# Kernel tuning notes

Measured on AMD Instinct MI355X. Metric: run time of the kernel, lower is better.

The kernel has to match this reference:

```python
import jax, jax.numpy as jnp
import numpy as np
from jax import lax

DIM = 180; NH = 6; WH = 16; WW = 16; MH = 8; MW = 8
HD = DIM // (2 * NH)  # 15, head dim; also the (non-sqrt) scale
RMS_EPS = 1.1920929e-07  # torch.finfo(float32).eps (RMSNorm eps=None)

def _conv(x, w, b, pad):
    # x: NHWC, w: HWIO
    return lax.conv_general_dilated(x, w, (1, 1), [(pad, pad), (pad, pad)],
                                    dimension_numbers=('NHWC', 'HWIO', 'NHWC')) + b

def _lrelu(x):
    return jnp.where(x >= 0, x, 0.2 * x)

def _ln(x, w, b, eps=1e-5):
    m = x.mean(-1, keepdims=True)
    v = jnp.mean((x - m) ** 2, -1, keepdims=True)
    return (x - m) / jnp.sqrt(v + eps) * w + b

def _forward(x, dfe_w1, dfe_b1, dfe_w2, dfe_b2, dfe_w3, dfe_b3, dfe_lw, dfe_lb,
             sl_w, sl_b, pos_pw, pos_pb, ln1w, ln1b, l1w, l1b, ln2w, ln2b,
             l2w, l2b, ln3w, ln3b, l3w, l3b, proj_w, proj_b, norm_w):
    B, C, H, W = x.shape
    xh = jnp.transpose(x, (0, 2, 3, 1))  # NHWC
    shortcut = xh
    # DFE: conv branch gated by 1x1 linear branch
    h = _lrelu(_conv(xh, dfe_w1, dfe_b1, 0))
    h = _lrelu(_conv(h, dfe_w2, dfe_b2, 1))
    h = _conv(h, dfe_w3, dfe_b3, 0)
    qv = h * _conv(xh, dfe_lw, dfe_lb, 0)  # (B,H,W,C)
    # window partition
    L = WH * WW
    qv = qv.reshape(B, H // WH, WH, W // WW, WW, C).transpose(0, 1, 3, 2, 4, 5).reshape(-1, L, C)
    Bw = qv.shape[0]
    qv = qv.reshape(Bw, L, 2, NH, HD).transpose(2, 0, 3, 1, 4)
    q, v = qv[0], qv[1]  # (Bw, NH, L, HD)
    # spatial linear projection of v: downsample window -> base window
    rH, rW = WH // MH, WW // MW
    vp = v.reshape(Bw, NH, MH, rH, MW, rW, HD).transpose(0, 1, 2, 4, 6, 3, 5)
    vp = vp.reshape(Bw, NH, MH * MW, HD, rH * rW)
    vp = ((vp @ sl_w) + sl_b)[..., 0]  # (Bw, NH, mapL, HD)
    corr = jnp.einsum('bhlc,bhmc->bhlm', q, vp) / HD  # (Bw, NH, L, mapL)
    # dynamic relative position bias
    bh = jnp.arange(1 - WH, WH, dtype=jnp.float32)
    bw = jnp.arange(1 - WW, WW, dtype=jnp.float32)
    biases = jnp.stack(jnp.meshgrid(bh, bw, indexing='ij')).reshape(2, -1).T  # (nb, 2)
    p = biases @ pos_pw + pos_pb
    p = jax.nn.relu(_ln(p, ln1w, ln1b)) @ l1w + l1b
    p = jax.nn.relu(_ln(p, ln2w, ln2b)) @ l2w + l2b
    pos = jax.nn.relu(_ln(p, ln3w, ln3b)) @ l3w + l3b  # (nb, NH)
    coords = jnp.stack(jnp.meshgrid(jnp.arange(WH), jnp.arange(WW), indexing='ij')).reshape(2, -1)
    rel = coords[:, :, None] - coords[:, None, :]  # (2, L, L)
    idx = (rel[0] + WH - 1) * (2 * WW - 1) + (rel[1] + WW - 1)  # (L, L)
    rpb = pos[idx.reshape(-1)].reshape(L, MH, rH, MW, rW, NH)
    rpb = rpb.transpose(0, 1, 3, 5, 2, 4).reshape(L, MH * MW, NH, rH * rW).mean(-1)
    rpb = rpb.transpose(2, 0, 1)  # (NH, L, mapL)
    corr = corr + rpb[None]
    xs = jnp.einsum('bhlm,bhmc->bhlc', corr, vp).transpose(0, 2, 1, 3).reshape(Bw, L, NH * HD)
    # channel self-correlation
    qc = q.transpose(0, 2, 1, 3).reshape(Bw, L, NH * HD)
    vc = v.transpose(0, 2, 1, 3).reshape(Bw, L, NH * HD)
    cmap = jnp.einsum('blc,bld->bcd', qc, vc) / L  # (Bw, C/2, C/2)
    xc = jnp.einsum('bcd,bld->blc', cmap, vc)  # (Bw, L, C/2)
    # window reverse
    def wrev(win):
        c = win.shape[-1]
        return win.reshape(B, H // WH, W // WW, WH, WW, c).transpose(0, 1, 3, 2, 4, 5).reshape(B, H, W, c)
    xs = wrev(xs.reshape(Bw, WH, WW, NH * HD))
    xc = wrev(xc.reshape(Bw, WH, WW, NH * HD))
    y = jnp.concatenate([xs, xc], -1)  # (B, H, W, C)
    y = y @ proj_w + proj_b
    y = y * (1.0 / jnp.sqrt(jnp.mean(y * y, -1, keepdims=True) + RMS_EPS)) * norm_w
    y = shortcut + y
    return jnp.transpose(y, (0, 3, 1, 2))


def setup_inputs() -> dict:
    key = jax.random.key(0)
    ks = iter(jax.random.split(key, 32))
    def rn(shape, s=0.05):
        return jax.random.normal(next(ks), shape, jnp.float32) * s
    inp = {}
    inp['x'] = jax.random.normal(next(ks), (4, 180, 256, 256), jnp.float32)
    inp['dfe_w1'] = rn((1, 1, 180, 36)); inp['dfe_b1'] = rn((36,))
    inp['dfe_w2'] = rn((3, 3, 36, 36)); inp['dfe_b2'] = rn((36,))
    inp['dfe_w3'] = rn((1, 1, 36, 180)); inp['dfe_b3'] = rn((180,))
    inp['dfe_lw'] = rn((1, 1, 180, 180)); inp['dfe_lb'] = rn((180,))
    inp['sl_w'] = rn((4, 1)); inp['sl_b'] = rn((1,))
    inp['pos_pw'] = rn((2, 11)); inp['pos_pb'] = rn((11,))
    inp['ln1w'] = jnp.ones((11,)); inp['ln1b'] = jnp.zeros((11,))
    inp['l1w'] = rn((11, 11)); inp['l1b'] = rn((11,))
    inp['ln2w'] = jnp.ones((11,)); inp['ln2b'] = jnp.zeros((11,))
    inp['l2w'] = rn((11, 11)); inp['l2b'] = rn((11,))
    inp['ln3w'] = jnp.ones((11,)); inp['ln3b'] = jnp.zeros((11,))
    inp['l3w'] = rn((11, 6)); inp['l3b'] = rn((6,))
    inp['proj_w'] = rn((180, 180)); inp['proj_b'] = rn((180,))
    inp['norm_w'] = jnp.ones((180,))
    return inp


def reference(x, dfe_w1, dfe_b1, dfe_w2, dfe_b2, dfe_w3, dfe_b3, dfe_lw, dfe_lb,
              sl_w, sl_b, pos_pw, pos_pb, ln1w, ln1b, l1w, l1b, ln2w, ln2b,
              l2w, l2b, ln3w, ln3b, l3w, l3b, proj_w, proj_b, norm_w):
    return _forward(x, dfe_w1, dfe_b1, dfe_w2, dfe_b2, dfe_w3, dfe_b3, dfe_lw, dfe_lb,
                    sl_w, sl_b, pos_pw, pos_pb, ln1w, ln1b, l1w, l1b, ln2w, ln2b,
                    l2w, l2b, ln3w, ln3b, l3w, l3b, proj_w, proj_b, norm_w)
```

## Files before the change

kernel.cpp:

```cpp
#include <hip/hip_runtime.h>
#include <stdint.h>

typedef unsigned short u16;
typedef unsigned int   u32;

#define HW 65536

typedef __bf16 bf16x8 __attribute__((ext_vector_type(8)));
typedef float  f32x4  __attribute__((ext_vector_type(4)));

static __device__ __forceinline__ float bf2f(u16 h) {
    u32 u = ((u32)h) << 16;
    return __builtin_bit_cast(float, u);
}
static __device__ __forceinline__ u16 f2bf(float f) {
    u32 u = __builtin_bit_cast(u32, f);
    u += 0x7fffu + ((u >> 16) & 1u);
    return (u16)(u >> 16);
}
static __device__ __forceinline__ void bf2x2(u32 u, float& a, float& b) {
    a = __builtin_bit_cast(float, u << 16);
    b = __builtin_bit_cast(float, u & 0xffff0000u);
}
static __device__ __forceinline__ f32x4 mfma16(bf16x8 a, bf16x8 b, f32x4 c) {
    return __builtin_amdgcn_mfma_f32_16x16x32_bf16(a, b, c, 0, 0, 0);
}

static __device__ __forceinline__ void lnrelu11(float* p, const float* __restrict__ w,
                                                const float* __restrict__ b) {
    float m = 0.f;
    #pragma unroll
    for (int k = 0; k < 11; k++) m += p[k];
    m *= (1.0f / 11.0f);
    float v = 0.f;
    #pragma unroll
    for (int k = 0; k < 11; k++) { float d = p[k] - m; v = fmaf(d, d, v); }
    v *= (1.0f / 11.0f);
    float r = 1.0f / sqrtf(v + 1e-5f);
    #pragma unroll
    for (int k = 0; k < 11; k++) {
        float t = (p[k] - m) * r * w[k] + b[k];
        p[k] = t > 0.f ? t : 0.f;
    }
}

__global__ __launch_bounds__(1024) void k_pos(
    const float* __restrict__ pw, const float* __restrict__ pb,
    const float* __restrict__ ln1w, const float* __restrict__ ln1b,
    const float* __restrict__ l1w, const float* __restrict__ l1b,
    const float* __restrict__ ln2w, const float* __restrict__ ln2b,
    const float* __restrict__ l2w, const float* __restrict__ l2b,
    const float* __restrict__ ln3w, const float* __restrict__ ln3b,
    const float* __restrict__ l3w, const float* __restrict__ l3b,
    float* __restrict__ pos)
{
    int i = threadIdx.x;
    if (i >= 961) return;
    float b0 = (float)(i / 31) - 15.0f;
    float b1 = (float)(i % 31) - 15.0f;
    float p[11], t[11];
    #pragma unroll
    for (int j = 0; j < 11; j++) p[j] = b0 * pw[j] + b1 * pw[11 + j] + pb[j];
    lnrelu11(p, ln1w, ln1b);
    #pragma unroll
    for (int j = 0; j < 11; j++) {
        float s = l1b[j];
        #pragma unroll
        for (int k = 0; k < 11; k++) s = fmaf(p[k], l1w[k * 11 + j], s);
        t[j] = s;
    }
    lnrelu11(t, ln2w, ln2b);
    #pragma unroll
    for (int j = 0; j < 11; j++) {
        float s = l2b[j];
        #pragma unroll
        for (int k = 0; k < 11; k++) s = fmaf(t[k], l2w[k * 11 + j], s);
        p[j] = s;
    }
    lnrelu11(p, ln3w, ln3b);
    #pragma unroll
    for (int h = 0; h < 6; h++) {
        float s = l3b[h];
        #pragma unroll
        for (int k = 0; k < 11; k++) s = fmaf(p[k], l3w[k * 6 + h], s);
        pos[i * 6 + h] = s;
    }
}

__global__ __launch_bounds__(256) void k_rpb(const float* __restrict__ pos,
                                             float* __restrict__ rpb)
{
    int g = blockIdx.x * 256 + threadIdx.x;
    if (g >= 6 * 256 * 64) return;
    int h = g >> 14;
    int l = (g >> 6) & 255;
    int m = g & 63;
    int yl = l >> 4, xl = l & 15;
    int my = m >> 3, mx = m & 7;
    float s = 0.f;
    #pragma unroll
    for (int ry = 0; ry < 2; ry++) {
        #pragma unroll
        for (int rx = 0; rx < 2; rx++) {
            int y2 = my * 2 + ry, x2 = mx * 2 + rx;
            int idx = (yl - y2 + 15) * 31 + (xl - x2 + 15);
            s += pos[idx * 6 + h];
        }
    }
    rpb[g] = 0.25f * s;
}

__global__ __launch_bounds__(256) void k_conv1(const float* __restrict__ x,
                                               const float* __restrict__ w,
                                               const float* __restrict__ b,
                                               u16* __restrict__ h1)
{
    int pix = blockIdx.x * 256 + threadIdx.x;
    int bb = pix >> 16, sp = pix & 65535;
    float acc[36];
    #pragma unroll
    for (int j = 0; j < 36; j++) acc[j] = b[j];
    const float* xp = x + (size_t)bb * 180 * HW + sp;
    for (int c = 0; c < 180; c++) {
        float xv = xp[(size_t)c * HW];
        #pragma unroll
        for (int j = 0; j < 36; j++) acc[j] = fmaf(xv, w[c * 36 + j], acc[j]);
    }
    u16* hp = h1 + (size_t)bb * 36 * HW + sp;
    #pragma unroll
    for (int j = 0; j < 36; j++) {
        float v = acc[j];
        v = v >= 0.f ? v : 0.2f * v;
        hp[(size_t)j * HW] = f2bf(v);
    }
}

__global__ __launch_bounds__(256) void k_conv3(const u16* __restrict__ h1,
                                               const float* __restrict__ w,
                                               const float* __restrict__ b,
                                               u16* __restrict__ h2)
{
    int tx = threadIdx.x, ty = threadIdx.y;
    int x0 = blockIdx.x * 16 + tx;
    int y0 = blockIdx.y * 16 + ty;
    int bb = blockIdx.z;
    float acc[36];
    #pragma unroll
    for (int j = 0; j < 36; j++) acc[j] = b[j];
    const u16* base = h1 + (size_t)bb * 36 * HW;
    for (int ky = 0; ky < 3; ky++) {
        int yy = y0 + ky - 1;
        if (yy < 0 || yy >= 256) continue;
        for (int kx = 0; kx < 3; kx++) {
            int xx = x0 + kx - 1;
            if (xx < 0 || xx >= 256) continue;
            const u16* ip = base + yy * 256 + xx;
            const float* wp = w + ((ky * 3 + kx) * 36) * 36;
            for (int c = 0; c < 36; c++) {
                float v = bf2f(ip[(size_t)c * HW]);
                #pragma unroll
                for (int j = 0; j < 36; j++) acc[j] = fmaf(v, wp[c * 36 + j], acc[j]);
            }
        }
    }
    u16* op = h2 + (size_t)bb * 36 * HW + y0 * 256 + x0;
    #pragma unroll
    for (int j = 0; j < 36; j++) {
        float v = acc[j];
        v = v >= 0.f ? v : 0.2f * v;
        op[(size_t)j * HW] = f2bf(v);
    }
}

__global__ __launch_bounds__(256) void k_wgprep(const float* __restrict__ lw,
                                                const float* __restrict__ w3,
                                                u16* __restrict__ gwh,
                                                u16* __restrict__ gwl,
                                                u16* __restrict__ cwh,
                                                u16* __restrict__ cwl)
{
    int gidx = blockIdx.x * 256 + threadIdx.x;
    if (gidx < 36864) {
        int oc = gidx / 192, k = gidx % 192;
        float v = (oc < 180 && k < 180) ? lw[k * 180 + oc] : 0.f;
        u16 h = f2bf(v);
        float lo = v - bf2f(h);
        gwh[gidx] = h;
        gwl[gidx] = f2bf(lo);
    } else {
        int r = gidx - 36864;
        int oc = r / 64, k = r % 64;
        float v = (oc < 180 && k < 36) ? w3[k * 180 + oc] : 0.f;
        u16 h = f2bf(v);
        float lo = v - bf2f(h);
        cwh[r] = h;
        cwl[r] = f2bf(lo);
    }
}

__global__ __launch_bounds__(256) void k_gate(const u16* __restrict__ h2,
                                              const float* __restrict__ x,
                                              const u16* __restrict__ gwh,
                                              const u16* __restrict__ gwl,
                                              const u16* __restrict__ cwh,
                                              const u16* __restrict__ cwl,
                                              const float* __restrict__ b3,
                                              const float* __restrict__ lb,
                                              u16* __restrict__ qvT)
{
    __shared__ __align__(16) float xs[180 * 64];
    __shared__ __align__(16) u16  hs[36 * 64];
    int t = threadIdx.x;
    int lane = t & 63;
    int g = __builtin_amdgcn_readfirstlane(t >> 6);
    int m = lane & 15, q = lane >> 4;
    int blk = blockIdx.x;
    int w  = blk >> 2;
    int lq = blk & 3;
    int bb = w >> 8, wy = (w >> 4) & 15, wx = w & 15;
    int ocb = g * 48;
    int y0 = wy * 16 + lq * 4;
    int xc0 = wx * 16;
    const float* xb = x + (size_t)bb * 180 * HW;
    const u16*  hb = h2 + (size_t)bb * 36 * HW;

    for (int s = g; s < 45; s += 4) {
        int c = s * 4 + (lane >> 4);
        int swz = (c >> 3) & 1;
        int pp = (lane & 15) ^ (swz << 2);
        int p0 = pp * 4;
        int prow = p0 >> 4, pcol = p0 & 15;
        const float* gp = xb + (size_t)c * HW + (y0 + prow) * 256 + xc0 + pcol;
        __builtin_amdgcn_global_load_lds(
            (const __attribute__((address_space(1))) void*)gp,
            (__attribute__((address_space(3))) void*)(xs + s * 256),
            16, 0, 0);
    }
    for (int idx = t; idx < 288; idx += 256) {
        int c = idx >> 3, j = idx & 7;
        int p0 = j * 8;
        int prow = p0 >> 4, pcol = p0 & 15;
        uint4 v = *(const uint4*)(hb + (size_t)c * HW + (y0 + prow) * 256 + xc0 + pcol);
        int swz = (c >> 3) & 1;
        *(uint4*)(hs + c * 64 + (p0 ^ (swz << 4))) = v;
    }
    __syncthreads();

    f32x4 accG[3][4], accC[3][4];
    #pragma unroll
    for (int mt = 0; mt < 3; mt++)
        #pragma unroll
        for (int pt = 0; pt < 4; pt++) {
            f32x4 z = {0.f, 0.f, 0.f, 0.f};
            accG[mt][pt] = z;
            accC[mt][pt] = z;
        }

    #pragma unroll 2
    for (int ks = 0; ks < 6; ks++) {
        bf16x8 Bh[4], Bl[4];
        #pragma unroll
        for (int pt = 0; pt < 4; pt++)
            #pragma unroll
            for (int j = 0; j < 8; j++) {
                int c = ks * 32 + q * 8 + j;
                if (c > 179) c = 179;
                int p = pt * 16 + m;
                float v = xs[c * 64 + (p ^ (((c >> 3) & 1) << 4))];
                __bf16 hi = (__bf16)v;
                Bh[pt][j] = hi;
                Bl[pt][j] = (__bf16)(v - (float)hi);
            }
        #pragma unroll
        for (int mt = 0; mt < 3; mt++) {
            bf16x8 Ah = *(const bf16x8*)(gwh + (size_t)(ocb + mt * 16 + m) * 192 + ks * 32 + q * 8);
            bf16x8 Al = *(const bf16x8*)(gwl + (size_t)(ocb + mt * 16 + m) * 192 + ks * 32 + q * 8);
            #pragma unroll
            for (int pt = 0; pt < 4; pt++) {
                accG[mt][pt] = mfma16(Ah, Bh[pt], accG[mt][pt]);
                accG[mt][pt] = mfma16(Al, Bh[pt], accG[mt][pt]);
                accG[mt][pt] = mfma16(Ah, Bl[pt], accG[mt][pt]);
            }
        }
    }

    #pragma unroll
    for (int ks = 0; ks < 2; ks++) {
        bf16x8 B[4];
        #pragma unroll
        for (int pt = 0; pt < 4; pt++)
            #pragma unroll
            for (int j = 0; j < 8; j++) {
                int c = ks * 32 + q * 8 + j;
                if (c > 35) c = 35;
                int p = pt * 16 + m;
                B[pt][j] = __builtin_bit_cast(__bf16, hs[c * 64 + (p ^ (((c >> 3) & 1) << 4))]);
            }
        #pragma unroll
        for (int mt = 0; mt < 3; mt++) {
            bf16x8 Ah = *(const bf16x8*)(cwh + (size_t)(ocb + mt * 16 + m) * 64 + ks * 32 + q * 8);
            bf16x8 Al = *(const bf16x8*)(cwl + (size_t)(ocb + mt * 16 + m) * 64 + ks * 32 + q * 8);
            #pragma unroll
            for (int pt = 0; pt < 4; pt++) {
                accC[mt][pt] = mfma16(Ah, B[pt], accC[mt][pt]);
                accC[mt][pt] = mfma16(Al, B[pt], accC[mt][pt]);
            }
        }
    }

    u16* qw = qvT + (size_t)w * 180 * 256 + lq * 64 + m;
    #pragma unroll
    for (int mt = 0; mt < 3; mt++)
        #pragma unroll
        for (int r = 0; r < 4; r++) {
            int oc = ocb + mt * 16 + q * 4 + r;
            if (oc < 180) {
                float bc = b3[oc], bg = lb[oc];
                #pragma unroll
                for (int pt = 0; pt < 4; pt++) {
                    float ah = accC[mt][pt][r] + bc;
                    float al = accG[mt][pt][r] + bg;
                    qw[(size_t)oc * 256 + pt * 16] = f2bf(ah * al);
                }
            }
        }
}

__global__ __launch_bounds__(256) void k_spat(const u16* __restrict__ qvT,
                                              const float* __restrict__ rpb,
                                              const float* __restrict__ slw,
                                              const float* __restrict__ slb,
                                              u16* __restrict__ yp)
{
    __shared__ __align__(16) float vp[6144];
    int w = blockIdx.x;
    int bb = w >> 8, wy = (w >> 4) & 15, wx = w & 15;
    int t = threadIdx.x;
    int lane = t & 63, wv = t >> 6;
    const u16* qw = qvT + (size_t)w * 180 * 256;
    float s0 = slw[0], s1 = slw[1], s2 = slw[2], s3 = slw[3], sb = slb[0];
    for (int o = t; o < 384; o += 256) vp[(o >> 6) * 1024 + (o & 63) * 16 + 15] = 0.f;
    for (int it = 0; it < 23; it++) {
        int p = wv + it * 4;
        if (p < 90) {
            int mm = lane;
            int l0 = (mm >> 3) * 32 + (mm & 7) * 2;
            const u16* rp2 = qw + (size_t)(90 + p) * 256;
            float s = sb + s0 * bf2f(rp2[l0]) + s1 * bf2f(rp2[l0 + 1])
                         + s2 * bf2f(rp2[l0 + 16]) + s3 * bf2f(rp2[l0 + 17]);
            vp[(p / 15) * 1024 + mm * 16 + (p % 15)] = s;
        }
    }
    __syncthreads();
    int l = t;
    size_t pixl = (size_t)((bb * 256 + wy * 16 + (l >> 4)) * 256 + wx * 16 + (l & 15));
    u16* op = yp + pixl * 192;
    ((u32*)op)[45] = 0u; ((u32*)op)[46] = 0u; ((u32*)op)[47] = 0u;
    for (int h = 0; h < 6; h++) {
        float q[16];
        #pragma unroll
        for (int d = 0; d < 15; d++) q[d] = bf2f(qw[(size_t)(h * 15 + d) * 256 + l]);
        q[15] = 0.f;
        float acc[16];
        #pragma unroll
        for (int d = 0; d < 16; d++) acc[d] = 0.f;
        const float* rp = rpb + ((h * 256 + l) << 6);
        const float4* vph = (const float4*)(vp + (h << 10));
        for (int m0 = 0; m0 < 64; m0 += 4) {
            float ra[4];
            *(float4*)ra = *(const float4*)(rp + m0);
            #pragma unroll
            for (int mm = 0; mm < 4; mm++) {
                int m = m0 + mm;
                float wvv[16];
                ((float4*)wvv)[0] = vph[m * 4 + 0];
                ((float4*)wvv)[1] = vph[m * 4 + 1];
                ((float4*)wvv)[2] = vph[m * 4 + 2];
                ((float4*)wvv)[3] = vph[m * 4 + 3];
                float s = 0.f;
                #pragma unroll
                for (int d2 = 0; d2 < 16; d2++) s = fmaf(q[d2], wvv[d2], s);
                s = s * (1.0f / 15.0f) + ra[mm];
                #pragma unroll
                for (int d2 = 0; d2 < 16; d2++) acc[d2] = fmaf(s, wvv[d2], acc[d2]);
            }
        }
        #pragma unroll
        for (int d = 0; d < 15; d++) op[h * 15 + d] = f2bf(acc[d]);
    }
}

__global__ __launch_bounds__(256) void k_chan(const u16* __restrict__ qvT,
                                              u16* __restrict__ yp)
{
    __shared__ __align__(16) u16 cm[96 * 104];
    __shared__ __align__(16) u16 xcb[128 * 104];
    int w = blockIdx.x;
    int bb = w >> 8, wy = (w >> 4) & 15, wx = w & 15;
    int t = threadIdx.x;
    int lane = t & 63, wv = t >> 6;
    int m = lane & 15, quad = lane >> 4;
    const u16* qw = qvT + (size_t)w * 180 * 256;

    int ct0 = (wv & 1) * 3, dt0 = (wv >> 1) * 3;
    f32x4 acc[3][3];
    #pragma unroll
    for (int i = 0; i < 3; i++)
        #pragma unroll
        for (int j = 0; j < 3; j++) {
            f32x4 z = {0.f, 0.f, 0.f, 0.f};
            acc[i][j] = z;
        }
    #pragma unroll
    for (int ks = 0; ks < 8; ks++) {
        bf16x8 A[3], B[3];
        #pragma unroll
        for (int i = 0; i < 3; i++)
            A[i] = *(const bf16x8*)(qw + (size_t)((ct0 + i) * 16 + m) * 256 + ks * 32 + quad * 8);
        #pragma unroll
        for (int j = 0; j < 3; j++) {
            int d = (dt0 + j) * 16 + m;
            int dd = d > 89 ? 89 : d;
            B[j] = *(const bf16x8*)(qw + (size_t)(90 + dd) * 256 + ks * 32 + quad * 8);
        }
        #pragma unroll
        for (int i = 0; i < 3; i++)
            #pragma unroll
            for (int j = 0; j < 3; j++)
                acc[i][j] = mfma16(A[i], B[j], acc[i][j]);
    }
    #pragma unroll
    for (int i = 0; i < 3; i++)
        #pragma unroll
        for (int j = 0; j < 3; j++)
            #pragma unroll
            for (int r = 0; r < 4; r++)
                cm[((ct0 + i) * 16 + quad * 4 + r) * 104 + (dt0 + j) * 16 + m] =
                    f2bf(acc[i][j][r] * (1.0f / 256.0f));
    __syncthreads();
    if (t < 96) {
        u32* z = (u32*)(cm + t * 104 + 90);
        z[0] = 0; z[1] = 0; z[2] = 0;
    }
    __syncthreads();

    int base_pix = (bb * 256 + wy * 16) * 256 + wx * 16;
    const __bf16* qwb = (const __bf16*)qw;
    for (int half = 0; half < 2; half++) {
        #pragma unroll
        for (int i = 0; i < 2; i++) {
            int ltl = wv * 2 + i;
            int lt = half * 8 + ltl;
            bf16x8 A[3];
            #pragma unroll
            for (int ks = 0; ks < 3; ks++) {
                const __bf16* colp = qwb + lt * 16 + m;
                #pragma unroll
                for (int j2 = 0; j2 < 8; j2++) {
                    int d = ks * 32 + quad * 8 + j2;
                    int dd = d > 89 ? 89 : d;
                    A[ks][j2] = colp[(size_t)(90 + dd) * 256];
                }
            }
            for (int ct = 0; ct < 6; ct++) {
                f32x4 c4 = {0.f, 0.f, 0.f, 0.f};
                #pragma unroll
                for (int ks = 0; ks < 3; ks++) {
                    bf16x8 B = *(const bf16x8*)(cm + (ct * 16 + m) * 104 + ks * 32 + quad * 8);
                    c4 = mfma16(A[ks], B, c4);
                }
                #pragma unroll
                for (int r = 0; r < 4; r++)
                    xcb[(ltl * 16 + quad * 4 + r) * 104 + ct * 16 + m] = f2bf(c4[r]);
            }
        }
        __syncthreads();
        #pragma unroll
        for (int it = 0; it < 6; it++) {
            int gg = t + it * 256;
            int lrow = gg / 12, seg = gg % 12;
            int l = half * 128 + lrow;
            int pix = base_pix + (l >> 4) * 256 + (l & 15);
            *(uint4*)(yp + (size_t)pix * 192 + 96 + seg * 8) =
                *(const uint4*)(xcb + lrow * 104 + seg * 8);
        }
        __syncthreads();
    }
}

__global__ __launch_bounds__(256) void k_wprep(const float* __restrict__ pjw,
                                               u16* __restrict__ whiT,
                                               u16* __restrict__ wloT)
{
    int g = blockIdx.x * 256 + threadIdx.x;
    int oc = g / 192, k = g % 192;
    int kp = -1;
    if (k < 90) kp = k;
    else if (k >= 96 && k <= 185) kp = k - 6;
    float v = (kp >= 0 && oc < 180) ? pjw[kp * 180 + oc] : 0.f;
    u16 h = f2bf(v);
    float lo = v - bf2f(h);
    whiT[g] = h;
    wloT[g] = f2bf(lo);
}

__global__ __launch_bounds__(256) void k_proj(const u16* __restrict__ yp,
                                              const float* __restrict__ x,
                                              const u16* __restrict__ whiT,
                                              const u16* __restrict__ wloT,
                                              const float* __restrict__ pb,
                                              const float* __restrict__ nw,
                                              float* __restrict__ out)
{
    __shared__ __align__(16) float st[96 * 68];
    __shared__ float part[4][4][16];
    int t = threadIdx.x;
    int lane = t & 63;
    int g = __builtin_amdgcn_readfirstlane(t >> 6);
    int m = lane & 15, q = lane >> 4;
    int pix0 = blockIdx.x * 64;
    int ocbase = g * 48;

    f32x4 acc[3][4];
    #pragma unroll
    for (int mt = 0; mt < 3; mt++)
        #pragma unroll
        for (int pt = 0; pt < 4; pt++) {
            f32x4 z = {0.f, 0.f, 0.f, 0.f};
            acc[mt][pt] = z;
        }

    const u16* bbase = yp + (size_t)pix0 * 192;
    #pragma unroll 2
    for (int ks = 0; ks < 6; ks++) {
        bf16x8 B[4];
        #pragma unroll
        for (int pt = 0; pt < 4; pt++)
            B[pt] = *(const bf16x8*)(bbase + (size_t)(pt * 16 + m) * 192 + ks * 32 + q * 8);
        #pragma unroll
        for (int mt = 0; mt < 3; mt++) {
            bf16x8 Ah = *(const bf16x8*)(whiT + (size_t)(ocbase + mt * 16 + m) * 192 + ks * 32 + q * 8);
            bf16x8 Al = *(const bf16x8*)(wloT + (size_t)(ocbase + mt * 16 + m) * 192 + ks * 32 + q * 8);
            #pragma unroll
            for (int pt = 0; pt < 4; pt++) {
                acc[mt][pt] = mfma16(Ah, B[pt], acc[mt][pt]);
                acc[mt][pt] = mfma16(Al, B[pt], acc[mt][pt]);
            }
        }
    }

    float pbv[3][4], nwv[3][4];
    #pragma unroll
    for (int mt = 0; mt < 3; mt++)
        #pragma unroll
        for (int r = 0; r < 4; r++) {
            int oc = ocbase + mt * 16 + q * 4 + r;
            bool ok = oc < 180;
            pbv[mt][r] = ok ? pb[oc] : 0.f;
            nwv[mt][r] = ok ? nw[oc] : 0.f;
        }
    float ss[4] = {0.f, 0.f, 0.f, 0.f};
    #pragma unroll
    for (int mt = 0; mt < 3; mt++)
        #pragma unroll
        for (int pt = 0; pt < 4; pt++)
            #pragma unroll
            for (int r = 0; r < 4; r++) {
                float y = acc[mt][pt][r] + pbv[mt][r];
                acc[mt][pt][r] = y;
                ss[pt] = fmaf(y, y, ss[pt]);
            }
    #pragma unroll
    for (int pt = 0; pt < 4; pt++) {
        ss[pt] += __shfl_xor(ss[pt], 16);
        ss[pt] += __shfl_xor(ss[pt], 32);
    }
    if (q == 0) {
        #pragma unroll
        for (int pt = 0; pt < 4; pt++) part[g][pt][m] = ss[pt];
    }
    __syncthreads();
    float scale[4];
    #pragma unroll
    for (int pt = 0; pt < 4; pt++) {
        float tot = part[0][pt][m] + part[1][pt][m] + part[2][pt][m] + part[3][pt][m];
        scale[pt] = 1.0f / sqrtf(tot * (1.0f / 180.0f) + 1.1920929e-7f);
    }
    #pragma unroll
    for (int mt = 0; mt < 3; mt++)
        #pragma unroll
        for (int pt = 0; pt < 4; pt++)
            #pragma unroll
            for (int r = 0; r < 4; r++)
                acc[mt][pt][r] = acc[mt][pt][r] * scale[pt] * nwv[mt][r];

    int bb = pix0 >> 16, sp0 = pix0 & 65535;
    const float* xb = x + (size_t)bb * 180 * HW + sp0;
    float* ob = out + (size_t)bb * 180 * HW + sp0;
    #pragma unroll
    for (int ph = 0; ph < 2; ph++) {
        if ((g >> 1) == ph) {
            int rb = (g & 1) * 48;
            #pragma unroll
            for (int mt = 0; mt < 3; mt++)
                #pragma unroll
                for (int r = 0; r < 4; r++) {
                    int row = rb + mt * 16 + q * 4 + r;
                    #pragma unroll
                    for (int pt = 0; pt < 4; pt++)
                        st[row * 68 + pt * 16 + m] = acc[mt][pt][r];
                }
        }
        __syncthreads();
        int nch = ph ? 1344 : 1536;
        for (int i = t; i < nch; i += 256) {
            int row = i >> 4, j = i & 15;
            int oc = ph * 96 + row;
            f32x4 d = *(const f32x4*)(st + row * 68 + j * 4);
            size_t off = (size_t)oc * HW + j * 4;
            f32x4 xv = *(const f32x4*)(xb + off);
            *(f32x4*)(ob + off) = d + xv;
        }
        __syncthreads();
    }
}

extern "C" void kernel_launch(void* const* d_in, const int* in_sizes, int n_in,
                              void* d_out, int out_size, void* d_ws, size_t ws_size,
                              hipStream_t stream)
{
    const float* x    = (const float*)d_in[0];
    const float* w1   = (const float*)d_in[1];
    const float* b1   = (const float*)d_in[2];
    const float* w2   = (const float*)d_in[3];
    const float* b2   = (const float*)d_in[4];
    const float* w3   = (const float*)d_in[5];
    const float* b3   = (const float*)d_in[6];
    const float* lw   = (const float*)d_in[7];
    const float* lb   = (const float*)d_in[8];
    const float* slw  = (const float*)d_in[9];
    const float* slb  = (const float*)d_in[10];
    const float* pw   = (const float*)d_in[11];
    const float* pb   = (const float*)d_in[12];
    const float* ln1w = (const float*)d_in[13];
    const float* ln1b = (const float*)d_in[14];
    const float* l1w  = (const float*)d_in[15];
    const float* l1b  = (const float*)d_in[16];
    const float* ln2w = (const float*)d_in[17];
    const float* ln2b = (const float*)d_in[18];
    const float* l2w  = (const float*)d_in[19];
    const float* l2b  = (const float*)d_in[20];
    const float* ln3w = (const float*)d_in[21];
    const float* ln3b = (const float*)d_in[22];
    const float* l3w  = (const float*)d_in[23];
    const float* l3b  = (const float*)d_in[24];
    const float* pjw  = (const float*)d_in[25];
    const float* pjb  = (const float*)d_in[26];
    const float* nw   = (const float*)d_in[27];
    float* out = (float*)d_out;

    char* ws = (char*)d_ws;
    float* pos = (float*)(ws + 0);
    float* rpb = (float*)(ws + 24576);
    u16*  h2  = (u16*)(ws + 417792);
    u16*  whiT = (u16*)(ws + 417792);
    u16*  wloT = (u16*)(ws + 417792 + 73728);
    u16*  h1  = (u16*)(ws + 19292160);
    u16*  qvT = (u16*)(ws + 19292160);
    u16*  yp  = (u16*)(ws + 113664000);
    u16*  gwh = (u16*)(ws + 113664000);
    u16*  gwl = (u16*)(ws + 113664000 + 73728);
    u16*  cwh = (u16*)(ws + 113664000 + 147456);
    u16*  cwl = (u16*)(ws + 113664000 + 172032);

    k_wgprep<<<dim3(192), dim3(256), 0, stream>>>(lw, w3, gwh, gwl, cwh, cwl);
    k_pos<<<dim3(1), dim3(1024), 0, stream>>>(pw, pb, ln1w, ln1b, l1w, l1b,
                                              ln2w, ln2b, l2w, l2b, ln3w, ln3b,
                                              l3w, l3b, pos);
    k_rpb<<<dim3(384), dim3(256), 0, stream>>>(pos, rpb);
    k_conv1<<<dim3(1024), dim3(256), 0, stream>>>(x, w1, b1, h1);
    k_conv3<<<dim3(16, 16, 4), dim3(16, 16), 0, stream>>>(h1, w2, b2, h2);
    k_gate<<<dim3(4096), dim3(256), 0, stream>>>(h2, x, gwh, gwl, cwh, cwl,
                                                 b3, lb, qvT);
    k_wprep<<<dim3(144), dim3(256), 0, stream>>>(pjw, whiT, wloT);
    k_spat<<<dim3(1024), dim3(256), 0, stream>>>(qvT, rpb, slw, slb, yp);
    k_chan<<<dim3(1024), dim3(256), 0, stream>>>(qvT, yp);
    k_proj<<<dim3(4096), dim3(256), 0, stream>>>(yp, x, whiT, wloT, pjb, nw, out);
}
```

Before: 1.048 ms.

## Stage qv stores through LDS and prefetch proj activations via global_load_lds

The DFE kernel now writes its gated output tile into shared memory first and then stores it to global memory as coalesced 16-byte vectors, replacing scattered 2-byte stores. The projection kernel loads its 64-pixel activation tile into LDS once using direct global-to-LDS loads with an XOR swizzle, then reads the MFMA B operands from LDS instead of strided global loads. This cuts uncoalesced global traffic and repeated fetches across the four waves. The cost is extra barriers and LDS reuse that must not conflict with the later staging buffer.

```diff
diff --git a/kernel.cpp b/kernel.cpp
--- a/kernel.cpp
+++ b/kernel.cpp
@@ -308,7 +308,8 @@
         }
     }
 
-    u16* qw = qvT + (size_t)w * 180 * 256 + lq * 64 + m;
+    __syncthreads();
+    u16* qtile = (u16*)xs;
     #pragma unroll
     for (int mt = 0; mt < 3; mt++)
         #pragma unroll
@@ -320,10 +321,17 @@
                 for (int pt = 0; pt < 4; pt++) {
                     float ah = accC[mt][pt][r] + bc;
                     float al = accG[mt][pt][r] + bg;
-                    qw[(size_t)oc * 256 + pt * 16] = f2bf(ah * al);
+                    qtile[oc * 66 + pt * 16 + m] = f2bf(ah * al);
                 }
             }
         }
+    __syncthreads();
+    u16* qbase = qvT + (size_t)w * 180 * 256 + lq * 64;
+    for (int i = t; i < 1440; i += 256) {
+        int oc = i >> 3, ch = i & 7;
+        *(uint4*)(qbase + (size_t)oc * 256 + ch * 8) =
+            *(const uint4*)(qtile + oc * 66 + ch * 8);
+    }
 }
 
 __global__ __launch_bounds__(256) void k_spat(const u16* __restrict__ qvT,
@@ -512,8 +520,10 @@
                                               const float* __restrict__ nw,
                                               float* __restrict__ out)
 {
-    __shared__ __align__(16) float st[96 * 68];
+    __shared__ __align__(16) char smem[26112];
     __shared__ float part[4][4][16];
+    u16*   ypl = (u16*)smem;
+    float* st  = (float*)smem;
     int t = threadIdx.x;
     int lane = t & 63;
     int g = __builtin_amdgcn_readfirstlane(t >> 6);
@@ -521,6 +531,16 @@
     int pix0 = blockIdx.x * 64;
     int ocbase = g * 48;
 
+    const char* ypc = (const char*)(yp + (size_t)pix0 * 192);
+    int soff = (lane ^ ((lane >> 3) & 7)) << 4;
+    for (int i = g; i < 24; i += 4) {
+        __builtin_amdgcn_global_load_lds(
+            (const __attribute__((address_space(1))) void*)(ypc + i * 1024 + soff),
+            (__attribute__((address_space(3))) void*)(smem + i * 1024),
+            16, 0, 0);
+    }
+    __syncthreads();
+
     f32x4 acc[3][4];
     #pragma unroll
     for (int mt = 0; mt < 3; mt++)
@@ -530,13 +550,17 @@
             acc[mt][pt] = z;
         }
 
-    const u16* bbase = yp + (size_t)pix0 * 192;
+    int mq = m * 24 + q;
     #pragma unroll 2
     for (int ks = 0; ks < 6; ks++) {
         bf16x8 B[4];
         #pragma unroll
-        for (int pt = 0; pt < 4; pt++)
-            B[pt] = *(const bf16x8*)(bbase + (size_t)(pt * 16 + m) * 192 + ks * 32 + q * 8);
+        for (int pt = 0; pt < 4; pt++) {
+            int G = pt * 384 + mq + ks * 4;
+            int o = G & 63;
+            int slot = (G & ~63) + (o ^ ((o >> 3) & 7));
+            B[pt] = *(const bf16x8*)(ypl + slot * 8);
+        }
         #pragma unroll
         for (int mt = 0; mt < 3; mt++) {
             bf16x8 Ah = *(const bf16x8*)(whiT + (size_t)(ocbase + mt * 16 + m) * 192 + ks * 32 + q * 8);
```

New measurement: 1.025 ms. 2.2% less time.
